# Optimization experiments

Hardware: AMD Instinct MI355X
Metric: run time of the kernel (lower is better)

## Reference

```python
import jax, jax.numpy as jnp
import numpy as np

VOCAB = 50257
N_EMBD = 640
BLOCK = 256
B = 16


def setup_inputs() -> dict:
    key = jax.random.key(0)
    ks = jax.random.split(key, 8)
    std = 0.02
    return {
        "idx": jax.random.randint(ks[0], (B, BLOCK), 0, VOCAB, dtype=jnp.int64 if jax.config.jax_enable_x64 else jnp.int32),
        "w_embed": jax.random.normal(ks[1], (VOCAB, N_EMBD), jnp.float32) * std,
        "w_pos": jax.random.normal(ks[2], (BLOCK, N_EMBD), jnp.float32) * std,
        "wq": jax.random.normal(ks[3], (N_EMBD, N_EMBD), jnp.float32) * std,
        "wk": jax.random.normal(ks[4], (N_EMBD, N_EMBD), jnp.float32) * std,
        "wv": jax.random.normal(ks[5], (N_EMBD, N_EMBD), jnp.float32) * std,
        "w_out": jax.random.normal(ks[6], (VOCAB, N_EMBD), jnp.float32) * std,
        "b_out": jnp.zeros((VOCAB,), jnp.float32),
    }


def reference(idx, w_embed, w_pos, wq, wk, wv, w_out, b_out):
    # idx: (B, T) token ids. Dropout is identity (eval mode).
    Bt, T = idx.shape
    x = w_embed[idx] + w_pos[:T]                      # (B, T, D)
    q = jnp.einsum('btd,ed->bte', x, wq)              # torch Linear: x @ W.T
    k = jnp.einsum('btd,ed->bte', x, wk)
    v = jnp.einsum('btd,ed->bte', x, wv)
    scale = jnp.asarray(N_EMBD ** 0.5, x.dtype)
    scores = jnp.einsum('btd,bsd->bts', q, k) / scale  # (B, T, T)
    causal = jnp.triu(jnp.ones((T, T), bool), k=1)     # True above diagonal
    scores = jnp.where(causal, jnp.asarray(-jnp.inf, scores.dtype), scores)
    attn = jax.nn.softmax(scores, axis=-1)
    attn_out = jnp.einsum('bts,bsd->btd', attn, v)     # (B, T, D)
    logits = jnp.einsum('btd,vd->btv', attn_out, w_out) + b_out  # (B, T, V)
    return logits
```

## Files before the change

kernel.cpp:

```cpp
#include <hip/hip_runtime.h>
#include <hip/hip_bf16.h>
#include <stdint.h>

#define VOCAB 50257
#define VPAD  50432
#define DIM   640
#define SEQ   256
#define NBATCH 16
#define MROWS 4096

using bf16 = __hip_bfloat16;
typedef __attribute__((ext_vector_type(8))) short short8;
typedef __attribute__((ext_vector_type(4))) float f32x4;
struct bf16x4 { bf16 a, b, c, d; };

__device__ __forceinline__ void gld_lds16(const void* g, void* l) {
  __builtin_amdgcn_global_load_lds(
      (const __attribute__((address_space(1))) void*)g,
      (__attribute__((address_space(3))) void*)l, 16, 0, 0);
}

#define BAR() asm volatile("s_barrier" ::: "memory")
#define VMC0() asm volatile("s_waitcnt vmcnt(0)" ::: "memory")

__global__ void embed_kernel(const int* __restrict__ idx,
                             const float* __restrict__ we,
                             const float* __restrict__ wp,
                             bf16* __restrict__ xb) {
  int row = blockIdx.x;
  int t = row & (SEQ - 1);
  int tok = idx[row];
  const float* src = we + (long)tok * DIM;
  const float* pos = wp + (long)t * DIM;
  for (int d = threadIdx.x * 4; d < DIM; d += blockDim.x * 4) {
    float4 s = *(const float4*)(src + d);
    float4 p = *(const float4*)(pos + d);
    bf16x4 o = { __float2bfloat16(s.x + p.x), __float2bfloat16(s.y + p.y),
                 __float2bfloat16(s.z + p.z), __float2bfloat16(s.w + p.w) };
    *(bf16x4*)(xb + (long)row * DIM + d) = o;
  }
}

__global__ void conv4_kernel(const float* __restrict__ src, bf16* __restrict__ dst,
                             long n_src, long n_dst) {
  long i = ((long)blockIdx.x * blockDim.x + threadIdx.x) * 4;
  long stride = (long)gridDim.x * blockDim.x * 4;
  for (; i < n_dst; i += stride) {
    float4 v = (i < n_src) ? *(const float4*)(src + i) : make_float4(0.f, 0.f, 0.f, 0.f);
    bf16x4 o = { __float2bfloat16(v.x), __float2bfloat16(v.y),
                 __float2bfloat16(v.z), __float2bfloat16(v.w) };
    *(bf16x4*)(dst + i) = o;
  }
}

__global__ void transpose_v(const bf16* __restrict__ v, bf16* __restrict__ vt) {
  long i = (long)blockIdx.x * blockDim.x + threadIdx.x;
  if (i >= (long)NBATCH * DIM * SEQ) return;
  int t = (int)(i & (SEQ - 1));
  long be = i >> 8;
  int e = (int)(be % DIM);
  int b = (int)(be / DIM);
  vt[i] = v[((long)b * SEQ + t) * DIM + e];
}

__global__ void softmax_kernel(const float* __restrict__ sc, bf16* __restrict__ p) {
  int wid = threadIdx.x >> 6, lane = threadIdx.x & 63;
  int row = blockIdx.x * 4 + wid;
  int t = row & (SEQ - 1);
  const float* srow = sc + (long)row * SEQ;
  const float rsc = 0.03952847075210474f;
  float v[4];
  float mx = -1e30f;
#pragma unroll
  for (int i = 0; i < 4; ++i) {
    int s = lane + 64 * i;
    v[i] = (s <= t) ? srow[s] * rsc : -1e30f;
    mx = fmaxf(mx, v[i]);
  }
#pragma unroll
  for (int off = 32; off; off >>= 1) mx = fmaxf(mx, __shfl_xor(mx, off, 64));
  float sum = 0.f;
#pragma unroll
  for (int i = 0; i < 4; ++i) {
    int s = lane + 64 * i;
    v[i] = (s <= t) ? __expf(v[i] - mx) : 0.f;
    sum += v[i];
  }
#pragma unroll
  for (int off = 32; off; off >>= 1) sum += __shfl_xor(sum, off, 64);
  float inv = 1.f / sum;
#pragma unroll
  for (int i = 0; i < 4; ++i)
    p[(long)row * SEQ + lane + 64 * i] = __float2bfloat16(v[i] * inv);
}

template <int NT, typename OUT_T, bool BIAS>
__global__ __launch_bounds__(256, 4) void gemm_pipe(
    const bf16* __restrict__ Ag, const bf16* __restrict__ Bg,
    OUT_T* __restrict__ Cg, const float* __restrict__ bias,
    int K, int ldc, int Nstore, long sA, long sB, long sC) {
  __shared__ __align__(16) char lds[32768];
  const int tid = threadIdx.x;
  const int lane = tid & 63, wv = tid >> 6;
  const int lr = lane & 15, h16 = lane >> 4;

  const int tm = blockIdx.x, tn = blockIdx.y, bz = blockIdx.z;
  const bf16* A = Ag + (long)bz * sA + (long)tm * 128 * K;
  const bf16* B = Bg + (long)bz * sB + (long)tn * 128 * K;

  int srcE[2], dstW[2];
#pragma unroll
  for (int j = 0; j < 2; ++j) {
    int d = j * 256 + tid;
    int b = d ^ ((d >> 3) & 3);
    srcE[j] = (b >> 2) * K + (b & 3) * 8;
    dstW[j] = (j * 256 + wv * 64) * 16;
  }
  const bf16* aS0 = A + srcE[0];
  const bf16* aS1 = A + srcE[1];
  const bf16* bS0 = B + srcE[0];
  const bf16* bS1 = B + srcE[1];
  auto STAGE = [&](int slot, int t) {
    int kOff = t * 32;
    gld_lds16(aS0 + kOff, lds + slot + dstW[0]);
    gld_lds16(aS1 + kOff, lds + slot + dstW[1]);
    gld_lds16(bS0 + kOff, lds + slot + 8192 + dstW[0]);
    gld_lds16(bS1 + kOff, lds + slot + 8192 + dstW[1]);
  };

  const int wr = (wv >> 1) * 64, wc = (wv & 1) * 64;
  int aoff[4], boff[4];
#pragma unroll
  for (int m = 0; m < 4; ++m) {
    int La = (wr + m * 16 + lr) * 64 + h16 * 16;
    aoff[m] = La ^ (((La >> 7) & 3) << 4);
    int Lb = (wc + m * 16 + lr) * 64 + h16 * 16;
    boff[m] = 8192 + (Lb ^ (((Lb >> 7) & 3) << 4));
  }

  f32x4 acc[4][4] = {};
  short8 a[4], b[4];

  STAGE(0, 0);
  VMC0();
  BAR();

#pragma unroll 2
  for (int t = 0; t < NT; ++t) {
    const int cur = (t & 1) * 16384;
    if (t + 1 < NT) STAGE(16384 - cur, t + 1);
#pragma unroll
    for (int m = 0; m < 4; ++m) a[m] = *(const short8*)(lds + cur + aoff[m]);
#pragma unroll
    for (int n = 0; n < 4; ++n) b[n] = *(const short8*)(lds + cur + boff[n]);
    __builtin_amdgcn_s_setprio(1);
#pragma unroll
    for (int m = 0; m < 4; ++m)
#pragma unroll
      for (int n = 0; n < 4; ++n)
        acc[m][n] = __builtin_amdgcn_mfma_f32_16x16x32_bf16(a[m], b[n], acc[m][n], 0, 0, 0);
    __builtin_amdgcn_s_setprio(0);
    if (t + 1 < NT) VMC0();
    BAR();
  }

  OUT_T* C = Cg + (long)bz * sC;
  const int crow0 = tm * 128 + wr + h16 * 4;
  const int ccol0 = tn * 128 + wc + lr;
#pragma unroll
  for (int m = 0; m < 4; ++m)
#pragma unroll
    for (int n = 0; n < 4; ++n) {
      int col = ccol0 + n * 16;
      if (col < Nstore) {
        float bv = BIAS ? bias[col] : 0.f;
#pragma unroll
        for (int j = 0; j < 4; ++j) {
          long row = crow0 + m * 16 + j;
          float val = acc[m][n][j] + bv;
          if constexpr (sizeof(OUT_T) == 2)
            C[row * ldc + col] = __float2bfloat16(val);
          else
            C[row * ldc + col] = val;
        }
      }
    }
}

extern "C" void kernel_launch(void* const* d_in, const int* in_sizes, int n_in,
                              void* d_out, int out_size, void* d_ws, size_t ws_size,
                              hipStream_t stream) {
  const int*   idx     = (const int*)d_in[0];
  const float* w_embed = (const float*)d_in[1];
  const float* w_pos   = (const float*)d_in[2];
  const float* wq      = (const float*)d_in[3];
  const float* wk      = (const float*)d_in[4];
  const float* wv      = (const float*)d_in[5];
  const float* w_out   = (const float*)d_in[6];
  const float* b_out   = (const float*)d_in[7];
  float* out = (float*)d_out;

  size_t off = 0;
  auto alloc = [&](size_t bytes) {
    void* p = (char*)d_ws + off;
    off += (bytes + 255) & ~(size_t)255;
    return p;
  };
  bf16* x_bf    = (bf16*)alloc((size_t)MROWS * DIM * 2);
  bf16* wqkv_bf = (bf16*)alloc((size_t)3 * DIM * DIM * 2);
  bf16* wout_bf = (bf16*)alloc((size_t)VPAD * DIM * 2);
  bf16* qkv     = (bf16*)alloc((size_t)3 * MROWS * DIM * 2);
  bf16* vT      = (bf16*)alloc((size_t)NBATCH * DIM * SEQ * 2);
  float* scores = (float*)alloc((size_t)NBATCH * SEQ * SEQ * 4);
  bf16* P       = (bf16*)alloc((size_t)NBATCH * SEQ * SEQ * 2);
  bf16* attn    = (bf16*)alloc((size_t)MROWS * DIM * 2);

  const long QKV_S = (long)MROWS * DIM;
  const long W_S   = (long)DIM * DIM;

  embed_kernel<<<MROWS, 256, 0, stream>>>(idx, w_embed, w_pos, x_bf);

  conv4_kernel<<<256, 256, 0, stream>>>(wq, wqkv_bf,           W_S, W_S);
  conv4_kernel<<<256, 256, 0, stream>>>(wk, wqkv_bf + W_S,     W_S, W_S);
  conv4_kernel<<<256, 256, 0, stream>>>(wv, wqkv_bf + 2 * W_S, W_S, W_S);
  conv4_kernel<<<2048, 256, 0, stream>>>(w_out, wout_bf, (long)VOCAB * DIM, (long)VPAD * DIM);

  gemm_pipe<20, bf16, false><<<dim3(MROWS / 128, DIM / 128, 3), 256, 0, stream>>>(
      x_bf, wqkv_bf, qkv, nullptr, DIM, DIM, DIM, 0, W_S, QKV_S);

  {
    long n = (long)NBATCH * DIM * SEQ;
    transpose_v<<<(int)((n + 255) / 256), 256, 0, stream>>>(qkv + 2 * QKV_S, vT);
  }

  gemm_pipe<20, float, false><<<dim3(SEQ / 128, SEQ / 128, NBATCH), 256, 0, stream>>>(
      qkv, qkv + QKV_S, scores, nullptr, DIM, SEQ, SEQ,
      (long)SEQ * DIM, (long)SEQ * DIM, (long)SEQ * SEQ);

  softmax_kernel<<<MROWS / 4, 256, 0, stream>>>(scores, P);

  gemm_pipe<8, bf16, false><<<dim3(SEQ / 128, DIM / 128, NBATCH), 256, 0, stream>>>(
      P, vT, attn, nullptr, SEQ, DIM, DIM,
      (long)SEQ * SEQ, (long)DIM * SEQ, (long)SEQ * DIM);

  gemm_pipe<20, float, true><<<dim3(MROWS / 128, VPAD / 128, 1), 256, 0, stream>>>(
      attn, wout_bf, out, b_out, DIM, VOCAB, VOCAB, 0, 0, 0);
}
```

Before: 607.5 us.

## Triple-buffer GEMM LDS pipeline and stage fp32 epilogue through LDS

Grows the GEMM shared-memory ring from two to three stages, issuing loads two k-steps ahead and waiting with a partial vmcnt, so global-to-LDS copies get more time to overlap the MFMA work. Launch bounds drop from 4 to 3 blocks per CU to make room for the larger LDS footprint. For fp32 outputs, including the large vocab projection, accumulators are first transposed through swizzled per-wave LDS tiles and then written as 16-byte vector stores, aiming to cut store-instruction count. The trade-offs are lower occupancy and extra LDS traffic in the epilogue. Each vector store now covers fewer contiguous bytes per row, and on the odd-stride vocab output those stores are not 16-byte aligned.

```diff
diff --git a/kernel.cpp b/kernel.cpp
--- a/kernel.cpp
+++ b/kernel.cpp
@@ -21,7 +21,7 @@
 }
 
 #define BAR() asm volatile("s_barrier" ::: "memory")
-#define VMC0() asm volatile("s_waitcnt vmcnt(0)" ::: "memory")
+#define VMC(n) asm volatile("s_waitcnt vmcnt(" #n ")" ::: "memory")
 
 __global__ void embed_kernel(const int* __restrict__ idx,
                              const float* __restrict__ we,
@@ -95,11 +95,11 @@
 }
 
 template <int NT, typename OUT_T, bool BIAS>
-__global__ __launch_bounds__(256, 4) void gemm_pipe(
+__global__ __launch_bounds__(256, 3) void gemm_pipe(
     const bf16* __restrict__ Ag, const bf16* __restrict__ Bg,
     OUT_T* __restrict__ Cg, const float* __restrict__ bias,
     int K, int ldc, int Nstore, long sA, long sB, long sC) {
-  __shared__ __align__(16) char lds[32768];
+  __shared__ __align__(16) char lds[49152];
   const int tid = threadIdx.x;
   const int lane = tid & 63, wv = tid >> 6;
   const int lr = lane & 15, h16 = lane >> 4;
@@ -142,13 +142,14 @@
   short8 a[4], b[4];
 
   STAGE(0, 0);
-  VMC0();
+  if (NT > 1) STAGE(16384, 1);
+  VMC(4);
   BAR();
 
-#pragma unroll 2
+#pragma unroll
   for (int t = 0; t < NT; ++t) {
-    const int cur = (t & 1) * 16384;
-    if (t + 1 < NT) STAGE(16384 - cur, t + 1);
+    const int cur = (t % 3) * 16384;
+    if (t + 2 < NT) STAGE(((t + 2) % 3) * 16384, t + 2);
 #pragma unroll
     for (int m = 0; m < 4; ++m) a[m] = *(const short8*)(lds + cur + aoff[m]);
 #pragma unroll
@@ -160,31 +161,72 @@
       for (int n = 0; n < 4; ++n)
         acc[m][n] = __builtin_amdgcn_mfma_f32_16x16x32_bf16(a[m], b[n], acc[m][n], 0, 0, 0);
     __builtin_amdgcn_s_setprio(0);
-    if (t + 1 < NT) VMC0();
+    if (t + 2 < NT) { VMC(4); }
+    else if (t + 1 < NT) { VMC(0); }
     BAR();
   }
 
-  OUT_T* C = Cg + (long)bz * sC;
-  const int crow0 = tm * 128 + wr + h16 * 4;
-  const int ccol0 = tn * 128 + wc + lr;
-#pragma unroll
-  for (int m = 0; m < 4; ++m)
+  if constexpr (sizeof(OUT_T) == 4) {
+    float* Cf = (float*)Cg + (long)bz * sC;
+    float bv[4];
 #pragma unroll
     for (int n = 0; n < 4; ++n) {
-      int col = ccol0 + n * 16;
-      if (col < Nstore) {
-        float bv = BIAS ? bias[col] : 0.f;
-#pragma unroll
-        for (int j = 0; j < 4; ++j) {
-          long row = crow0 + m * 16 + j;
-          float val = acc[m][n][j] + bv;
-          if constexpr (sizeof(OUT_T) == 2)
-            C[row * ldc + col] = __float2bfloat16(val);
-          else
-            C[row * ldc + col] = val;
+      int col = tn * 128 + wc + lr + n * 16;
+      bv[n] = (BIAS && col < Nstore) ? bias[col] : 0.f;
+    }
+    char* reg = lds + wv * 8192;
+    const int rowL = lane & 31, cb = lane >> 5;
+#pragma unroll
+    for (int mm = 0; mm < 2; ++mm) {
+#pragma unroll
+      for (int mp = 0; mp < 2; ++mp)
+#pragma unroll
+        for (int n = 0; n < 4; ++n) {
+          f32x4 v = acc[mm * 2 + mp][n];
+          v[0] += bv[n]; v[1] += bv[n]; v[2] += bv[n]; v[3] += bv[n];
+          int col = lr + n * 16;
+          int rho = mp * 16 + h16 * 4;
+          int w = col * 32 + (rho ^ ((col & 7) << 2));
+          *(f32x4*)(reg + w * 4) = v;
+        }
+      const long rowg = tm * 128 + wr + mm * 32 + rowL;
+#pragma unroll
+      for (int k = 0; k < 8; ++k) {
+        f32x4 o;
+#pragma unroll
+        for (int c = 0; c < 4; ++c) {
+          int col = k * 8 + cb * 4 + c;
+          int w = col * 32 + (rowL ^ ((col & 7) << 2));
+          o[c] = *(const float*)(reg + w * 4);
+        }
+        int gcol = tn * 128 + wc + k * 8 + cb * 4;
+        if (gcol + 3 < Nstore) {
+          *(f32x4*)(Cf + rowg * (long)ldc + gcol) = o;
+        } else {
+#pragma unroll
+          for (int c = 0; c < 4; ++c)
+            if (gcol + c < Nstore) Cf[rowg * (long)ldc + gcol + c] = o[c];
         }
       }
     }
+  } else {
+    OUT_T* C = Cg + (long)bz * sC;
+    const int crow0 = tm * 128 + wr + h16 * 4;
+    const int ccol0 = tn * 128 + wc + lr;
+#pragma unroll
+    for (int m = 0; m < 4; ++m)
+#pragma unroll
+      for (int n = 0; n < 4; ++n) {
+        int col = ccol0 + n * 16;
+        if (col < Nstore) {
+#pragma unroll
+          for (int j = 0; j < 4; ++j) {
+            long row = crow0 + m * 16 + j;
+            C[row * ldc + col] = __float2bfloat16(acc[m][n][j]);
+          }
+        }
+      }
+  }
 }
 
 extern "C" void kernel_launch(void* const* d_in, const int* in_sizes, int n_in,
```

Result: slower. 635.7 us (+4.6%).
